# Performance work log

Measured on AMD Instinct MI355X. Metric: run time of the kernel, lower is better.

## Reference

```python
import jax, jax.numpy as jnp
import numpy as np

B, DIM, H, W = 8, 128, 112, 112
WSZ, K = 7, 9
D4 = DIM // 4


def setup_inputs() -> dict:
    key = jax.random.key(0)
    ks = jax.random.split(key, 8)
    w = lambda k, shape: jax.random.normal(k, shape, jnp.float32) * 0.05
    return {
        'x_in': jax.random.normal(ks[0], (B, DIM, H, W), jnp.float32),
        'f_w': w(ks[1], (D4, DIM)), 'f_b': jnp.zeros((D4,), jnp.float32),
        'f_gn_w': jnp.ones((D4,), jnp.float32), 'f_gn_b': jnp.zeros((D4,), jnp.float32),
        'p_w': w(ks[2], (DIM, D4)), 'p_b': jnp.zeros((DIM,), jnp.float32),
        'p_gn_w': jnp.ones((DIM,), jnp.float32), 'p_gn_b': jnp.zeros((DIM,), jnp.float32),
        'r_w': w(ks[3], (DIM, DIM)), 'r_b': jnp.zeros((DIM,), jnp.float32),
        'r_gn_w': jnp.ones((DIM,), jnp.float32), 'r_gn_b': jnp.zeros((DIM,), jnp.float32),
        'e1_w': w(ks[4], (D4, 2 * D4)), 'e1_b': jnp.zeros((D4,), jnp.float32),
        'e2_w': w(ks[5], (1, D4)), 'e2_b': jnp.zeros((1,), jnp.float32),
        'gamma': jnp.ones((1,), jnp.float32), 'beta': jnp.zeros((1,), jnp.float32),
    }


def conv1x1(x, w, b):
    # 1x1 conv == channel matmul. x: (B,C,H,W), w: (O,C)
    return jnp.einsum('bchw,oc->bohw', x, w) + b[None, :, None, None]


def gn1(x, w, b, eps=1e-5):
    # GroupNorm(1, C): normalize over (C,H,W) per sample
    mu = x.mean(axis=(1, 2, 3), keepdims=True)
    var = x.var(axis=(1, 2, 3), keepdims=True)
    xn = (x - mu) * jax.lax.rsqrt(var + eps)
    return xn * w[None, :, None, None] + b[None, :, None, None]


def reference(x_in, f_w, f_b, f_gn_w, f_gn_b, p_w, p_b, p_gn_w, p_gn_b,
              r_w, r_b, r_gn_w, r_gn_b, e1_w, e1_b, e2_w, e2_b, gamma, beta):
    b, c, h, w_ = x_in.shape
    wg = hg = WSZ
    pw, ph = h // wg, w_ // hg  # per-window spatial dims (16,16)

    residual = gn1(conv1x1(x_in, r_w, r_b), r_gn_w, r_gn_b)

    # 'b c (Wg w) (Hg h) -> (b Wg Hg) c w h'
    x = x_in.reshape(b, c, wg, pw, hg, ph).transpose(0, 2, 4, 1, 3, 5)
    x = x.reshape(b * wg * hg, c, pw, ph)

    f = gn1(conv1x1(x, f_w, f_b), f_gn_w, f_gn_b)  # (Bp, D4, pw, ph)
    bp, c4, hp, wp = f.shape
    n = hp * wp

    xf = f.reshape(bp, c4, n).transpose(0, 2, 1)  # (Bp, N, C4) nodes

    gy, gx = jnp.meshgrid(jnp.arange(hp), jnp.arange(wp), indexing='ij')
    grid = jnp.stack([gy, gx], axis=-1).astype(jnp.float32).reshape(n, 2)
    grid = (grid - grid.mean(0)) / (grid.std(0, ddof=1) + 1e-5)  # torch std is unbiased

    xa = jnp.concatenate([xf, jnp.broadcast_to(grid, (bp, n, 2))], axis=-1)
    xn = xa / jnp.maximum(jnp.linalg.norm(xa, axis=-1, keepdims=True), 1e-8)
    sim = jnp.einsum('bnd,bmd->bnm', xn, xn)  # (Bp, N, N) cosine sim
    sim = jnp.where(jnp.eye(n, dtype=bool), -jnp.inf, sim)
    _, topk_idx = jax.lax.top_k(sim, K)  # (Bp, N, K)

    # gather neighbor messages; scatter_add back to row == sum over K (rows are dense)
    msg = jax.vmap(lambda a, i: a[i])(xf, topk_idx)          # (Bp, N, K, C4)
    src = jnp.broadcast_to(xf[:, :, None, :], msg.shape)      # (Bp, N, K, C4)
    ef = jnp.concatenate([src, msg], axis=-1)                 # (Bp, N, K, 2*C4)
    h1 = jax.nn.silu(ef @ e1_w.T + e1_b)
    wgt = jax.nn.sigmoid(h1 @ e2_w.T + e2_b)[..., 0]          # (Bp, N, K)
    out = (msg * wgt[..., None]).sum(axis=2)                  # (Bp, N, C4)

    out = out * gamma + xf * beta
    out = out.reshape(bp, hp, wp, c4).transpose(0, 3, 1, 2)   # (Bp, C4, hp, wp)

    # '(b Wg Hg) c w h -> b c (Wg w) (Hg h)'
    out = out.reshape(b, wg, hg, c4, hp, wp).transpose(0, 3, 1, 4, 2, 5)
    out = out.reshape(b, c4, h, w_)

    out = gn1(conv1x1(out, p_w, p_b), p_gn_w, p_gn_b) + residual
    return out
```

## Files before the change

### kernel.cpp

```cpp
#include <hip/hip_runtime.h>
#include <hip/hip_fp16.h>
#include <math.h>

#define CIN 128
#define C4  32
#define HW  12544
#define KNB 9
#define NWIN 392

__device__ inline double wave_sum(double v) {
#pragma unroll
    for (int off = 32; off; off >>= 1) v += __shfl_down(v, off);
    return v;
}

#define TOP9_INSERT(sv, mi, tv, ti)                                  \
    {                                                                \
        _Pragma("unroll")                                            \
        for (int j = KNB - 1; j >= 1; --j) {                         \
            bool cj  = (sv) > tv[j];                                 \
            bool cjm = (sv) > tv[j - 1];                             \
            tv[j] = cj ? (cjm ? tv[j - 1] : (sv)) : tv[j];           \
            ti[j] = cj ? (cjm ? ti[j - 1] : (mi)) : ti[j];           \
        }                                                            \
        bool c0 = (sv) > tv[0];                                      \
        tv[0] = c0 ? (sv) : tv[0];                                   \
        ti[0] = c0 ? (mi) : ti[0];                                   \
    }

__global__ __launch_bounds__(256) void prep_kernel(
    const float* __restrict__ f_w, const float* __restrict__ r_w,
    const float* __restrict__ p_w,
    double* __restrict__ fw64t, float* __restrict__ rwt_t, float* __restrict__ pwt_t)
{
    const int i = blockIdx.x * 256 + threadIdx.x;
    if (i < 4096)  fw64t[(i & 127) * 32 + (i >> 7)]  = (double)f_w[i];
    if (i < 16384) rwt_t[(i & 127) * 128 + (i >> 7)] = r_w[i];
    if (i < 4096)  pwt_t[(i & 31) * 128 + (i >> 5)]  = p_w[i];
}

__global__ __launch_bounds__(512, 6) void fconv_rstats_kernel(
    const float* __restrict__ x_in,
    const double* __restrict__ fw64t, const float* __restrict__ f_b,
    const float* __restrict__ f_gn_w, const float* __restrict__ f_gn_b,
    const float* __restrict__ rwt_t, const float* __restrict__ r_b,
    double* __restrict__ xf64, double* __restrict__ invnws,
    double* __restrict__ stats)
{
    __shared__ __align__(16) char smem[34944];
    double* vbuf = (double*)smem;
    double* red  = (double*)(smem + 34816);
    const int t = threadIdx.x;

    if (blockIdx.x < NWIN) {
        const int win = blockIdx.x;
        const int b = win / 49, wg = (win / 7) % 7, hg = win % 7;
        const int n = t & 255, s = t >> 8;
        const int py = n >> 4, px = n & 15;
        const int rs = __builtin_amdgcn_readfirstlane(s);

        const float* xb = x_in + (size_t)b * CIN * HW + (size_t)(wg * 16 + py) * 112 + (hg * 16 + px);
        const double* wB = fw64t + 16 * rs;
        double acc[16];
#pragma unroll
        for (int j = 0; j < 16; ++j) acc[j] = 0.0;
#pragma unroll 2
        for (int c = 0; c < CIN; ++c) {
            double xv = (double)xb[(size_t)c * HW];
            const double* wr = wB + c * 32;
#pragma unroll
            for (int j = 0; j < 16; ++j) acc[j] = fma(wr[j], xv, acc[j]);
        }
        double s1 = 0.0, s2 = 0.0;
#pragma unroll
        for (int j = 0; j < 16; ++j) {
            double v = acc[j] + (double)f_b[16 * rs + j];
            acc[j] = v; s1 += v; s2 += v * v;
        }
        s1 = wave_sum(s1); s2 = wave_sum(s2);
        {
            int w = t >> 6;
            if ((t & 63) == 0) { red[w] = s1; red[8 + w] = s2; }
        }
        __syncthreads();
        double rs1 = 0.0, rs2 = 0.0;
#pragma unroll
        for (int w = 0; w < 8; ++w) { rs1 += red[w]; rs2 += red[8 + w]; }
        const double mu   = rs1 * (1.0 / 8192.0);
        const double var  = rs2 * (1.0 / 8192.0) - mu * mu;
        const double rstd = 1.0 / sqrt(var + 1e-5);

        float myv[16];
#pragma unroll
        for (int j = 0; j < 16; ++j) {
            int c = 16 * rs + j;
            myv[j] = (float)((acc[j] - mu) * rstd * (double)f_gn_w[c] + (double)f_gn_b[c]);
        }
        double* xrow = xf64 + (size_t)(win * 256 + n) * 34;
#pragma unroll
        for (int j2 = 0; j2 < 8; ++j2) {
            double2 d2 = { (double)myv[2 * j2], (double)myv[2 * j2 + 1] };
            ((double2*)(xrow + 16 * rs))[j2] = d2;
        }
        const double ginv = 1.0 / (sqrt(5440.0 / 255.0) + 1e-5);
        const float gyf = (float)(((double)py - 7.5) * ginv);
        const float gxf = (float)(((double)px - 7.5) * ginv);
        if (s == 0) {
            double2 g2 = { (double)gyf, (double)gxf };
            ((double2*)(xrow + 32))[0] = g2;
        }
        if (s == 1) {
#pragma unroll
            for (int j = 0; j < 16; ++j) vbuf[n * 17 + j] = (double)myv[j];
        }
        __syncthreads();
        if (s == 0) {
            double nrm = 0.0;
#pragma unroll
            for (int j = 0; j < 16; ++j) { double x = (double)myv[j]; nrm += x * x; }
#pragma unroll
            for (int j = 0; j < 16; ++j) { double x = vbuf[n * 17 + j]; nrm += x * x; }
            double xg = (double)gyf; nrm += xg * xg;
            double xh = (double)gxf; nrm += xh * xh;
            invnws[win * 256 + n] = 1.0 / fmax(sqrt(nrm), 1e-8);
        }
    } else {
        const int idx = blockIdx.x - NWIN;
        const int b = idx / 98, rem = idx % 98;
        const int oc = rem / 49, pg = rem % 49;
        const int sh = t >> 8, n = t & 255;
        const int rsh = __builtin_amdgcn_readfirstlane(sh);
        const float* wR = rwt_t + oc * 64 + rsh * 32;
        const float* xb = x_in + (size_t)b * CIN * HW + pg * 256 + n;
        float acc[32];
#pragma unroll
        for (int o = 0; o < 32; ++o) acc[o] = r_b[oc * 64 + rsh * 32 + o];
#pragma unroll 2
        for (int c = 0; c < CIN; ++c) {
            float xv = xb[(size_t)c * HW];
            const float* wr = wR + c * 128;
#pragma unroll
            for (int o = 0; o < 32; ++o) acc[o] = fmaf(wr[o], xv, acc[o]);
        }
        double s1 = 0.0, s2 = 0.0;
#pragma unroll
        for (int o = 0; o < 32; ++o) { double v = (double)acc[o]; s1 += v; s2 += v * v; }
        s1 = wave_sum(s1); s2 = wave_sum(s2);
        {
            int w = t >> 6;
            if ((t & 63) == 0) { red[w] = s1; red[8 + w] = s2; }
        }
        __syncthreads();
        if (t == 0) {
            double a = 0.0, c = 0.0;
#pragma unroll
            for (int w = 0; w < 8; ++w) { a += red[w]; c += red[8 + w]; }
            atomicAdd(&stats[b * 4 + 0], a);
            atomicAdd(&stats[b * 4 + 1], c);
        }
    }
}

__global__ __launch_bounds__(256, 4) void sim_hm_kernel(
    const double* __restrict__ xf64, const double* __restrict__ invnws,
    const float* __restrict__ e1_w,
    float* __restrict__ pval, unsigned char* __restrict__ pidx,
    __half* __restrict__ hmws)
{
    const int bid = blockIdx.x;
    if (bid < 2 * NWIN) {
        const int win = bid >> 1, m0 = (bid & 1) << 7;
        const int n = threadIdx.x;

        double xad[34];
        {
            const double2* own = (const double2*)(xf64 + (size_t)(win * 256 + n) * 34);
#pragma unroll
            for (int q = 0; q < 17; ++q) {
                double2 d = own[q];
                xad[2 * q] = d.x; xad[2 * q + 1] = d.y;
            }
        }
        const double inv_self = invnws[(size_t)win * 256 + n];
        const double* xmb  = xf64 + (size_t)(win * 256 + m0) * 34;
        const double* invb = invnws + (size_t)win * 256 + m0;

        float tv[KNB]; int ti[KNB];
#pragma unroll
        for (int k = 0; k < KNB; ++k) { tv[k] = -INFINITY; ti[k] = 0; }
#pragma unroll 2
        for (int mm = 0; mm < 128; ++mm) {
            const double* xm = xmb + mm * 34;
            double d0 = 0.0, d1 = 0.0, d2 = 0.0, d3 = 0.0;
#pragma unroll
            for (int q = 0; q < 8; ++q) {
                d0 = fma(xm[4 * q + 0], xad[4 * q + 0], d0);
                d1 = fma(xm[4 * q + 1], xad[4 * q + 1], d1);
                d2 = fma(xm[4 * q + 2], xad[4 * q + 2], d2);
                d3 = fma(xm[4 * q + 3], xad[4 * q + 3], d3);
            }
            d0 = fma(xm[32], xad[32], d0);
            d1 = fma(xm[33], xad[33], d1);
            double d = (d0 + d1) + (d2 + d3);
            float sv = (float)(d * (inv_self * invb[mm]));
            sv = (m0 + mm == n) ? -INFINITY : sv;
            TOP9_INSERT(sv, m0 + mm, tv, ti);
        }
        const size_t base = ((size_t)bid * 256 + n) * 9;
#pragma unroll
        for (int k = 0; k < KNB; ++k) { pval[base + k] = tv[k]; pidx[base + k] = (unsigned char)ti[k]; }
    } else {
        const int idxm = bid - 2 * NWIN;
        const int win = idxm >> 1, half = idxm & 1;
        const int t = threadIdx.x;
        const int n = t & 127;
        const int jh = __builtin_amdgcn_readfirstlane(t >> 7);
        const int gn = half * 128 + n;
        const double2* xr2 = (const double2*)(xf64 + (size_t)(win * 256 + gn) * 34);
        float xr[32];
#pragma unroll
        for (int q = 0; q < 16; ++q) {
            double2 d = xr2[q];
            xr[2 * q] = (float)d.x; xr[2 * q + 1] = (float)d.y;
        }
        __align__(16) __half hv[16];
#pragma unroll
        for (int jj = 0; jj < 16; ++jj) {
            const float* w = e1_w + (16 * jh + jj) * 64 + 32;
            float a = 0.f;
#pragma unroll
            for (int c = 0; c < C4; ++c) a = fmaf(w[c], xr[c], a);
            hv[jj] = __float2half_rn(a);
        }
        float4* dst = (float4*)(hmws + (size_t)(win * 256 + gn) * 32 + 16 * jh);
        dst[0] = ((const float4*)hv)[0];
        dst[1] = ((const float4*)hv)[1];
    }
}

__global__ __launch_bounds__(512, 6) void merge_mlp_kernel(
    const double* __restrict__ xf64, const __half* __restrict__ hmws,
    const float* __restrict__ pval, const unsigned char* __restrict__ pidx,
    const float* __restrict__ e1_w, const float* __restrict__ e1_b,
    const float* __restrict__ e2_w, const float* __restrict__ e2_b,
    const float* __restrict__ gamma, const float* __restrict__ beta,
    float* __restrict__ gnn)
{
    __shared__ __align__(16) char smem[50432];
    __half2* xf2 = (__half2*)smem;
    __half2* hm2 = (__half2*)(smem + 17408);
    __half2* hs2 = (__half2*)(smem + 34816);
    short*   Ti  = (short*)(smem + 43520);
    float*   Wt  = (float*)(smem + 45824);

    const int bid = blockIdx.x;
    const int win = bid >> 1, half = bid & 1;
    const int b = win / 49, wg = (win / 7) % 7, hg = win % 7;
    const int t = threadIdx.x;
    const int nl = t & 127, s = t >> 7;
    const int gn = half * 128 + nl;
    const int rs = __builtin_amdgcn_readfirstlane(s);

    {
        const int r = t >> 1, hh = t & 1;
        const double2* sx = (const double2*)(xf64 + (size_t)win * 256 * 34 + r * 34 + hh * 16);
#pragma unroll
        for (int q = 0; q < 4; ++q) {
            double2 a = sx[2 * q], b2 = sx[2 * q + 1];
            xf2[r * 17 + hh * 8 + 2 * q]     = __floats2half2_rn((float)a.x, (float)a.y);
            xf2[r * 17 + hh * 8 + 2 * q + 1] = __floats2half2_rn((float)b2.x, (float)b2.y);
        }
        const uint4* sh = (const uint4*)(hmws + (size_t)win * 8192 + r * 32 + hh * 16);
        uint4 u0 = sh[0], u1 = sh[1];
        unsigned int* d = (unsigned int*)(hm2 + r * 17 + hh * 8);
        d[0] = u0.x; d[1] = u0.y; d[2] = u0.z; d[3] = u0.w;
        d[4] = u1.x; d[5] = u1.y; d[6] = u1.z; d[7] = u1.w;
    }
    __syncthreads();

    {
        float xr[C4];
#pragma unroll
        for (int q = 0; q < 16; ++q) {
            float2 f = __half22float2(xf2[gn * 17 + q]);
            xr[2 * q] = f.x; xr[2 * q + 1] = f.y;
        }
        float hsv[8];
#pragma unroll
        for (int jj = 0; jj < 8; ++jj) {
            const int j = 8 * rs + jj;
            const float* w = e1_w + j * 64;
            float h0 = e1_b[j], h1 = 0.f;
#pragma unroll
            for (int c = 0; c < C4; c += 2) {
                h0 = fmaf(w[c], xr[c], h0);
                h1 = fmaf(w[c + 1], xr[c + 1], h1);
            }
            hsv[jj] = h0 + h1;
        }
#pragma unroll
        for (int u = 0; u < 4; ++u)
            hs2[nl * 17 + 4 * rs + u] = __floats2half2_rn(hsv[2 * u], hsv[2 * u + 1]);
    }
    if (s == 0) {
        float tv[KNB]; int ti[KNB];
#pragma unroll
        for (int k = 0; k < KNB; ++k) { tv[k] = -INFINITY; ti[k] = 0; }
        for (int qd = 0; qd < 2; ++qd) {
            const size_t base = ((size_t)(win * 2 + qd) * 256 + gn) * 9;
#pragma unroll
            for (int k = 0; k < KNB; ++k) {
                float sv = pval[base + k];
                int   mi = (int)pidx[base + k];
                TOP9_INSERT(sv, mi, tv, ti);
            }
        }
#pragma unroll
        for (int k = 0; k < KNB; ++k) Ti[nl * 9 + k] = (short)ti[k];
    }
    __syncthreads();

    {
        float hsr[C4];
#pragma unroll
        for (int q = 0; q < 16; ++q) {
            float2 f = __half22float2(hs2[nl * 17 + q]);
            hsr[2 * q] = f.x; hsr[2 * q + 1] = f.y;
        }
        const float e2b = e2_b[0];
        for (int k = s; k < KNB; k += 4) {
            const int m = (int)Ti[nl * 9 + k];
            float a2 = 0.f;
#pragma unroll
            for (int jp = 0; jp < 16; ++jp) {
                float2 hv = __half22float2(hm2[m * 17 + jp]);
                float h0 = hsr[2 * jp] + hv.x;
                float h1 = hsr[2 * jp + 1] + hv.y;
                float sg0 = 1.f / (1.f + __expf(-h0));
                a2 = fmaf(e2_w[2 * jp], h0 * sg0, a2);
                float sg1 = 1.f / (1.f + __expf(-h1));
                a2 = fmaf(e2_w[2 * jp + 1], h1 * sg1, a2);
            }
            Wt[nl * 9 + k] = 1.f / (1.f + __expf(-(a2 + e2b)));
        }
    }
    __syncthreads();

    {
        short tis[KNB]; float wks[KNB];
#pragma unroll
        for (int k = 0; k < KNB; ++k) { tis[k] = Ti[nl * 9 + k]; wks[k] = Wt[nl * 9 + k]; }
        const float g = gamma[0], be = beta[0];
        const int py = gn >> 4, px = gn & 15;
        float* gp = gnn + (size_t)b * C4 * HW + (size_t)(wg * 16 + py) * 112 + (hg * 16 + px);
        float xo[8];
#pragma unroll
        for (int q = 0; q < 4; ++q) {
            float2 f = __half22float2(xf2[gn * 17 + 4 * rs + q]);
            xo[2 * q] = f.x; xo[2 * q + 1] = f.y;
        }
        float o[8];
#pragma unroll
        for (int cc = 0; cc < 8; ++cc) o[cc] = 0.f;
#pragma unroll
        for (int k = 0; k < KNB; ++k) {
            const int mrow = (int)tis[k] * 17 + 4 * rs;
#pragma unroll
            for (int q = 0; q < 4; ++q) {
                float2 mv = __half22float2(xf2[mrow + q]);
                o[2 * q]     = fmaf(wks[k], mv.x, o[2 * q]);
                o[2 * q + 1] = fmaf(wks[k], mv.y, o[2 * q + 1]);
            }
        }
#pragma unroll
        for (int cc = 0; cc < 8; ++cc) {
            float gl = fmaf(g, o[cc], be * xo[cc]);
            gp[(size_t)(8 * rs + cc) * HW] = gl;
        }
    }
}

__global__ __launch_bounds__(256, 8) void pstats_kernel(
    const float* __restrict__ gnn, const float* __restrict__ p_w,
    const float* __restrict__ p_b, double* __restrict__ stats)
{
    __shared__ double red[16];
    const int idx = blockIdx.x;
    const int b = idx / 98, pg = idx % 98;
    const int t = threadIdx.x;
    const int pix = pg * 128 + (t & 127);
    const int oh = __builtin_amdgcn_readfirstlane(t >> 7);

    const float* gb = gnn + (size_t)b * C4 * HW + pix;
    float g[C4];
#pragma unroll
    for (int c = 0; c < C4; ++c) g[c] = gb[(size_t)c * HW];

    double s1 = 0.0, s2 = 0.0;
    const float* pwb = p_w + (size_t)oh * 64 * C4;
#pragma unroll 4
    for (int o = 0; o < 64; ++o) {
        const float* w = pwb + o * C4;
        float y = p_b[oh * 64 + o];
#pragma unroll
        for (int c = 0; c < C4; ++c) y = fmaf(w[c], g[c], y);
        s1 += (double)y; s2 += (double)y * (double)y;
    }
    s1 = wave_sum(s1); s2 = wave_sum(s2);
    {
        int w = t >> 6;
        if ((t & 63) == 0) { red[w] = s1; red[8 + w] = s2; }
    }
    __syncthreads();
    if (t == 0) {
        double a = 0.0, c = 0.0;
#pragma unroll
        for (int w = 0; w < 4; ++w) { a += red[w]; c += red[8 + w]; }
        atomicAdd(&stats[b * 4 + 2], a);
        atomicAdd(&stats[b * 4 + 3], c);
    }
}

__global__ __launch_bounds__(256) void final_kernel(
    const float* __restrict__ x_in, const float* __restrict__ gnn,
    const float* __restrict__ rwt_t, const float* __restrict__ r_b,
    const float* __restrict__ r_gn_w, const float* __restrict__ r_gn_b,
    const float* __restrict__ pwt_t, const float* __restrict__ p_b,
    const float* __restrict__ p_gn_w, const float* __restrict__ p_gn_b,
    const double* __restrict__ stats,
    float* __restrict__ out)
{
    const int idx = blockIdx.x;
    const int b = idx / 196, rem = idx % 196;
    const int ocq = rem / 49, pg = rem % 49;
    const int t = threadIdx.x;

    const double NN = (double)CIN * HW;
    const double mu_r = stats[b * 4 + 0] / NN;
    const float  rs_r = (float)(1.0 / sqrt(stats[b * 4 + 1] / NN - mu_r * mu_r + 1e-5));
    const double mu_p = stats[b * 4 + 2] / NN;
    const float  rs_p = (float)(1.0 / sqrt(stats[b * 4 + 3] / NN - mu_p * mu_p + 1e-5));
    const float fmur = (float)mu_r, fmup = (float)mu_p;

    const int p = pg * 256 + t;
    const float* xb = x_in + (size_t)b * CIN * HW + p;
    const float* gb = gnn + (size_t)b * C4 * HW + p;
    float* ob = out + (size_t)b * CIN * HW + p;

    float xg[C4];
#pragma unroll
    for (int c = 0; c < C4; ++c) xg[c] = gb[(size_t)c * HW];

    float accR[32], accP[32];
#pragma unroll
    for (int o = 0; o < 32; ++o) {
        accR[o] = r_b[ocq * 32 + o];
        accP[o] = p_b[ocq * 32 + o];
    }
#pragma unroll 2
    for (int c = 0; c < CIN; ++c) {
        float xv = xb[(size_t)c * HW];
        const float* w = rwt_t + c * 128 + ocq * 32;
#pragma unroll
        for (int o = 0; o < 32; ++o) accR[o] = fmaf(w[o], xv, accR[o]);
    }
#pragma unroll
    for (int c = 0; c < C4; ++c) {
        const float* w = pwt_t + c * 128 + ocq * 32;
#pragma unroll
        for (int o = 0; o < 32; ++o) accP[o] = fmaf(w[o], xg[c], accP[o]);
    }
#pragma unroll
    for (int o = 0; o < 32; ++o) {
        const int O = ocq * 32 + o;
        float yr = (accR[o] - fmur) * rs_r * r_gn_w[O] + r_gn_b[O];
        float yp = (accP[o] - fmup) * rs_p * p_gn_w[O] + p_gn_b[O];
        ob[(size_t)O * HW] = yp + yr;
    }
}

extern "C" void kernel_launch(void* const* d_in, const int* in_sizes, int n_in,
                              void* d_out, int out_size, void* d_ws, size_t ws_size,
                              hipStream_t stream)
{
    const float* x_in   = (const float*)d_in[0];
    const float* f_w    = (const float*)d_in[1];
    const float* f_b    = (const float*)d_in[2];
    const float* f_gn_w = (const float*)d_in[3];
    const float* f_gn_b = (const float*)d_in[4];
    const float* p_w    = (const float*)d_in[5];
    const float* p_b    = (const float*)d_in[6];
    const float* p_gn_w = (const float*)d_in[7];
    const float* p_gn_b = (const float*)d_in[8];
    const float* r_w    = (const float*)d_in[9];
    const float* r_b    = (const float*)d_in[10];
    const float* r_gn_w = (const float*)d_in[11];
    const float* r_gn_b = (const float*)d_in[12];
    const float* e1_w   = (const float*)d_in[13];
    const float* e1_b   = (const float*)d_in[14];
    const float* e2_w   = (const float*)d_in[15];
    const float* e2_b   = (const float*)d_in[16];
    const float* gamma  = (const float*)d_in[17];
    const float* beta   = (const float*)d_in[18];

    char* wsb = (char*)d_ws;
    float*         gnn    = (float*)        (wsb + 0);
    double*        stats  = (double*)       (wsb + 12845056);
    double*        invnws = (double*)       (wsb + 12845312);
    float*         pval   = (float*)        (wsb + 13648128);
    unsigned char* pidx   = (unsigned char*)(wsb + 20873472);
    double*        fw64t  = (double*)       (wsb + 22679808);
    float*         rwt_t  = (float*)        (wsb + 22712576);
    float*         pwt_t  = (float*)        (wsb + 22778112);
    __half*        hmws   = (__half*)       (wsb + 22794496);
    double*        xf64   = (double*)       (wsb + 29217024);

    hipMemsetAsync(stats, 0, 32 * sizeof(double), stream);
    prep_kernel<<<64, 256, 0, stream>>>(f_w, r_w, p_w, fw64t, rwt_t, pwt_t);
    fconv_rstats_kernel<<<NWIN + 784, 512, 0, stream>>>(
        x_in, fw64t, f_b, f_gn_w, f_gn_b, rwt_t, r_b, xf64, invnws, stats);
    sim_hm_kernel<<<NWIN * 2 + NWIN * 2, 256, 0, stream>>>(
        xf64, invnws, e1_w, pval, pidx, hmws);
    merge_mlp_kernel<<<NWIN * 2, 512, 0, stream>>>(
        xf64, hmws, pval, pidx, e1_w, e1_b, e2_w, e2_b, gamma, beta, gnn);
    pstats_kernel<<<784, 256, 0, stream>>>(gnn, p_w, p_b, stats);
    final_kernel<<<1568, 256, 0, stream>>>(
        x_in, gnn, rwt_t, r_b, r_gn_w, r_gn_b, pwt_t, p_b, p_gn_w, p_gn_b, stats, (float*)d_out);
}
```

Before: 338.0 us.

## Fold weight prep into fconv and move residual stats into sim kernel

```diff
diff --git a/kernel.cpp b/kernel.cpp
--- a/kernel.cpp
+++ b/kernel.cpp
@@ -14,10 +14,10 @@
     return v;
 }
 
-#define TOP9_INSERT(sv, mi, tv, ti)                                  \
+#define TOPK_INSERT(K, sv, mi, tv, ti)                               \
     {                                                                \
         _Pragma("unroll")                                            \
-        for (int j = KNB - 1; j >= 1; --j) {                         \
+        for (int j = (K) - 1; j >= 1; --j) {                         \
             bool cj  = (sv) > tv[j];                                 \
             bool cjm = (sv) > tv[j - 1];                             \
             tv[j] = cj ? (cjm ? tv[j - 1] : (sv)) : tv[j];           \
@@ -28,48 +28,50 @@
         ti[0] = c0 ? (mi) : ti[0];                                   \
     }
 
-__global__ __launch_bounds__(256) void prep_kernel(
-    const float* __restrict__ f_w, const float* __restrict__ r_w,
-    const float* __restrict__ p_w,
-    double* __restrict__ fw64t, float* __restrict__ rwt_t, float* __restrict__ pwt_t)
-{
-    const int i = blockIdx.x * 256 + threadIdx.x;
-    if (i < 4096)  fw64t[(i & 127) * 32 + (i >> 7)]  = (double)f_w[i];
-    if (i < 16384) rwt_t[(i & 127) * 128 + (i >> 7)] = r_w[i];
-    if (i < 4096)  pwt_t[(i & 31) * 128 + (i >> 5)]  = p_w[i];
-}
-
-__global__ __launch_bounds__(512, 6) void fconv_rstats_kernel(
+__global__ __launch_bounds__(512, 2) void fconv_prep_kernel(
     const float* __restrict__ x_in,
-    const double* __restrict__ fw64t, const float* __restrict__ f_b,
+    const float* __restrict__ f_w, const float* __restrict__ f_b,
     const float* __restrict__ f_gn_w, const float* __restrict__ f_gn_b,
-    const float* __restrict__ rwt_t, const float* __restrict__ r_b,
+    const float* __restrict__ r_w, const float* __restrict__ p_w,
     double* __restrict__ xf64, double* __restrict__ invnws,
-    double* __restrict__ stats)
+    float* __restrict__ rwt_t, float* __restrict__ pwt_t)
 {
     __shared__ __align__(16) char smem[34944];
-    double* vbuf = (double*)smem;
-    double* red  = (double*)(smem + 34816);
     const int t = threadIdx.x;
 
     if (blockIdx.x < NWIN) {
+        double* wbufd = (double*)smem;
+        double* vbuf  = (double*)smem;
+        double* red   = (double*)(smem + 34816);
         const int win = blockIdx.x;
         const int b = win / 49, wg = (win / 7) % 7, hg = win % 7;
         const int n = t & 255, s = t >> 8;
         const int py = n >> 4, px = n & 15;
         const int rs = __builtin_amdgcn_readfirstlane(s);
 
+        for (int i = t; i < C4 * CIN; i += 512) {
+            int o = i >> 7, c = i & 127;
+            wbufd[(c >> 1) * 64 + o * 2 + (c & 1)] = (double)f_w[i];
+        }
+        __syncthreads();
+
         const float* xb = x_in + (size_t)b * CIN * HW + (size_t)(wg * 16 + py) * 112 + (hg * 16 + px);
-        const double* wB = fw64t + 16 * rs;
         double acc[16];
 #pragma unroll
         for (int j = 0; j < 16; ++j) acc[j] = 0.0;
-#pragma unroll 2
-        for (int c = 0; c < CIN; ++c) {
-            double xv = (double)xb[(size_t)c * HW];
-            const double* wr = wB + c * 32;
-#pragma unroll
-            for (int j = 0; j < 16; ++j) acc[j] = fma(wr[j], xv, acc[j]);
+        {
+            const double2* wrow = (const double2*)wbufd + 16 * rs;
+            for (int c2 = 0; c2 < 64; ++c2) {
+                double xv0 = (double)xb[(size_t)(2 * c2) * HW];
+                double xv1 = (double)xb[(size_t)(2 * c2 + 1) * HW];
+                const double2* wr = wrow + c2 * 32;
+#pragma unroll
+                for (int j = 0; j < 16; ++j) {
+                    double2 w2 = wr[j];
+                    acc[j] = fma(w2.x, xv0, acc[j]);
+                    acc[j] = fma(w2.y, xv1, acc[j]);
+                }
+            }
         }
         double s1 = 0.0, s2 = 0.0;
 #pragma unroll
@@ -125,48 +127,21 @@
             invnws[win * 256 + n] = 1.0 / fmax(sqrt(nrm), 1e-8);
         }
     } else {
-        const int idx = blockIdx.x - NWIN;
-        const int b = idx / 98, rem = idx % 98;
-        const int oc = rem / 49, pg = rem % 49;
-        const int sh = t >> 8, n = t & 255;
-        const int rsh = __builtin_amdgcn_readfirstlane(sh);
-        const float* wR = rwt_t + oc * 64 + rsh * 32;
-        const float* xb = x_in + (size_t)b * CIN * HW + pg * 256 + n;
-        float acc[32];
-#pragma unroll
-        for (int o = 0; o < 32; ++o) acc[o] = r_b[oc * 64 + rsh * 32 + o];
-#pragma unroll 2
-        for (int c = 0; c < CIN; ++c) {
-            float xv = xb[(size_t)c * HW];
-            const float* wr = wR + c * 128;
-#pragma unroll
-            for (int o = 0; o < 32; ++o) acc[o] = fmaf(wr[o], xv, acc[o]);
-        }
-        double s1 = 0.0, s2 = 0.0;
-#pragma unroll
-        for (int o = 0; o < 32; ++o) { double v = (double)acc[o]; s1 += v; s2 += v * v; }
-        s1 = wave_sum(s1); s2 = wave_sum(s2);
-        {
-            int w = t >> 6;
-            if ((t & 63) == 0) { red[w] = s1; red[8 + w] = s2; }
-        }
-        __syncthreads();
-        if (t == 0) {
-            double a = 0.0, c = 0.0;
-#pragma unroll
-            for (int w = 0; w < 8; ++w) { a += red[w]; c += red[8 + w]; }
-            atomicAdd(&stats[b * 4 + 0], a);
-            atomicAdd(&stats[b * 4 + 1], c);
-        }
-    }
-}
-
-__global__ __launch_bounds__(256, 4) void sim_hm_kernel(
+        const int i = (blockIdx.x - NWIN) * 512 + t;
+        if (i < 16384) rwt_t[(i & 127) * 128 + (i >> 7)] = r_w[i];
+        if (i < 4096)  pwt_t[(i & 31) * 128 + (i >> 5)]  = p_w[i];
+    }
+}
+
+__global__ __launch_bounds__(256, 2) void sim_hm_rstats_kernel(
+    const float* __restrict__ x_in,
     const double* __restrict__ xf64, const double* __restrict__ invnws,
     const float* __restrict__ e1_w,
+    const float* __restrict__ rwt_t, const float* __restrict__ r_b,
     float* __restrict__ pval, unsigned char* __restrict__ pidx,
-    __half* __restrict__ hmws)
+    __half* __restrict__ hmws, double* __restrict__ stats)
 {
+    __shared__ double red[16];
     const int bid = blockIdx.x;
     if (bid < 2 * NWIN) {
         const int win = bid >> 1, m0 = (bid & 1) << 7;
@@ -204,12 +179,12 @@
             double d = (d0 + d1) + (d2 + d3);
             float sv = (float)(d * (inv_self * invb[mm]));
             sv = (m0 + mm == n) ? -INFINITY : sv;
-            TOP9_INSERT(sv, m0 + mm, tv, ti);
+            TOPK_INSERT(KNB, sv, m0 + mm, tv, ti);
         }
         const size_t base = ((size_t)bid * 256 + n) * 9;
 #pragma unroll
         for (int k = 0; k < KNB; ++k) { pval[base + k] = tv[k]; pidx[base + k] = (unsigned char)ti[k]; }
-    } else {
+    } else if (bid < 4 * NWIN) {
         const int idxm = bid - 2 * NWIN;
         const int win = idxm >> 1, half = idxm & 1;
         const int t = threadIdx.x;
@@ -235,6 +210,41 @@
         float4* dst = (float4*)(hmws + (size_t)(win * 256 + gn) * 32 + 16 * jh);
         dst[0] = ((const float4*)hv)[0];
         dst[1] = ((const float4*)hv)[1];
+    } else {
+        const int idx = bid - 4 * NWIN;
+        const int b = idx / 49, pg = idx % 49;
+        const int t = threadIdx.x;
+        const float* xb = x_in + (size_t)b * CIN * HW + pg * 256 + t;
+        double s1 = 0.0, s2 = 0.0;
+#pragma unroll 1
+        for (int pass = 0; pass < 4; ++pass) {
+            const int o0 = pass * 32;
+            float acc[32];
+#pragma unroll
+            for (int o = 0; o < 32; ++o) acc[o] = r_b[o0 + o];
+#pragma unroll 2
+            for (int c = 0; c < CIN; ++c) {
+                float xv = xb[(size_t)c * HW];
+                const float* wr = rwt_t + c * 128 + o0;
+#pragma unroll
+                for (int o = 0; o < 32; ++o) acc[o] = fmaf(wr[o], xv, acc[o]);
+            }
+#pragma unroll
+            for (int o = 0; o < 32; ++o) { double v = (double)acc[o]; s1 += v; s2 += v * v; }
+        }
+        s1 = wave_sum(s1); s2 = wave_sum(s2);
+        {
+            int w = t >> 6;
+            if ((t & 63) == 0) { red[w] = s1; red[8 + w] = s2; }
+        }
+        __syncthreads();
+        if (t == 0) {
+            double a = 0.0, c = 0.0;
+#pragma unroll
+            for (int w = 0; w < 4; ++w) { a += red[w]; c += red[8 + w]; }
+            atomicAdd(&stats[b * 4 + 0], a);
+            atomicAdd(&stats[b * 4 + 1], c);
+        }
     }
 }
 
@@ -312,7 +322,7 @@
             for (int k = 0; k < KNB; ++k) {
                 float sv = pval[base + k];
                 int   mi = (int)pidx[base + k];
-                TOP9_INSERT(sv, mi, tv, ti);
+                TOPK_INSERT(KNB, sv, mi, tv, ti);
             }
         }
 #pragma unroll
@@ -509,18 +519,16 @@
     double*        invnws = (double*)       (wsb + 12845312);
     float*         pval   = (float*)        (wsb + 13648128);
     unsigned char* pidx   = (unsigned char*)(wsb + 20873472);
-    double*        fw64t  = (double*)       (wsb + 22679808);
-    float*         rwt_t  = (float*)        (wsb + 22712576);
-    float*         pwt_t  = (float*)        (wsb + 22778112);
-    __half*        hmws   = (__half*)       (wsb + 22794496);
-    double*        xf64   = (double*)       (wsb + 29217024);
+    float*         rwt_t  = (float*)        (wsb + 22679808);
+    float*         pwt_t  = (float*)        (wsb + 22745344);
+    __half*        hmws   = (__half*)       (wsb + 22761728);
+    double*        xf64   = (double*)       (wsb + 29184256);
 
     hipMemsetAsync(stats, 0, 32 * sizeof(double), stream);
-    prep_kernel<<<64, 256, 0, stream>>>(f_w, r_w, p_w, fw64t, rwt_t, pwt_t);
-    fconv_rstats_kernel<<<NWIN + 784, 512, 0, stream>>>(
-        x_in, fw64t, f_b, f_gn_w, f_gn_b, rwt_t, r_b, xf64, invnws, stats);
-    sim_hm_kernel<<<NWIN * 2 + NWIN * 2, 256, 0, stream>>>(
-        xf64, invnws, e1_w, pval, pidx, hmws);
+    fconv_prep_kernel<<<NWIN + 32, 512, 0, stream>>>(
+        x_in, f_w, f_b, f_gn_w, f_gn_b, r_w, p_w, xf64, invnws, rwt_t, pwt_t);
+    sim_hm_rstats_kernel<<<NWIN * 2 + NWIN * 2 + NWIN, 256, 0, stream>>>(
+        x_in, xf64, invnws, e1_w, rwt_t, r_b, pval, pidx, hmws, stats);
     merge_mlp_kernel<<<NWIN * 2, 512, 0, stream>>>(
         xf64, hmws, pval, pidx, e1_w, e1_b, e2_w, e2_b, gamma, beta, gnn);
     pstats_kernel<<<784, 256, 0, stream>>>(gnn, p_w, p_b, stats);
```

Measured after the change: 377.8 us. 1.12x slower.
